# Optimization experiments

Measured on AMD Instinct MI355X. Metric: run time of the kernel, lower is better.

The kernel has to match this reference:

```python
import jax, jax.numpy as jnp
import numpy as np
from jax import lax

LEVELS = 3
K = 8  # db4 filter length
DEC_LO = jnp.asarray([-0.0105974018, 0.0328830117, 0.0308413818, -0.1870348117,
                      -0.0279837694, 0.6308807679, 0.7148465706, 0.2303778133], dtype=jnp.float32)
DEC_HI = jnp.asarray([-0.2303778133, 0.7148465706, -0.6308807679, -0.0279837694,
                      0.1870348117, 0.0308413818, -0.0328830117, -0.0105974018], dtype=jnp.float32)
REC_LO = jnp.asarray([0.2303778133, 0.7148465706, 0.6308807679, -0.0279837694,
                      -0.1870348117, 0.0308413818, 0.0328830117, -0.0105974018], dtype=jnp.float32)
REC_HI = jnp.asarray([-0.0105974018, -0.0328830117, 0.0308413818, 0.1870348117,
                      -0.0279837694, -0.6308807679, 0.7148465706, -0.2303778133], dtype=jnp.float32)
DN = ('NCH', 'OIH', 'NCH')


def _dwconv_stride2(x, w):
    # depthwise conv1d, stride 2, symmetric (reflect) pad of K-1 on both sides.
    # Same filter for every channel -> fold channels into batch for a single-filter conv.
    B, C, L = x.shape
    xp = jnp.pad(x, ((0, 0), (0, 0), (K - 1, K - 1)), mode='reflect')
    out = lax.conv_general_dilated(xp.reshape(B * C, 1, -1), w.reshape(1, 1, K),
                                   window_strides=(2,), padding='VALID',
                                   dimension_numbers=DN)
    return out.reshape(B, C, -1)


def _dwconvT_stride2(x, w):
    # depthwise conv_transpose1d, stride 2 == lhs-dilated conv with flipped kernel,
    # padding K-1 on both sides. Output length = 2*L + K - 2 (matches torch).
    B, C, L = x.shape
    out = lax.conv_general_dilated(x.reshape(B * C, 1, L), w[::-1].reshape(1, 1, K),
                                   window_strides=(1,), padding=[(K - 1, K - 1)],
                                   lhs_dilation=(2,), dimension_numbers=DN)
    return out.reshape(B, C, -1)


def _fit(out, target_len):
    # center-crop if too long, right-zero-pad if too short (as in torch code)
    L = out.shape[-1]
    if L > target_len:
        s = (L - target_len) // 2
        return out[..., s:s + target_len]
    if L < target_len:
        return jnp.pad(out, ((0, 0), (0, 0), (0, target_len - L)))
    return out


def setup_inputs() -> dict:
    key = jax.random.key(0)
    x = jax.random.normal(key, (16, 128, 8192), dtype=jnp.float32)
    return {"x": x}


def reference(x):
    # Multi-level analysis
    approx = x
    details = []
    target_lens = []
    for _ in range(LEVELS):
        target_lens.append(approx.shape[-1])
        details.append(_dwconv_stride2(approx, DEC_HI))
        approx = _dwconv_stride2(approx, DEC_LO)
    L0 = x.shape[-1]

    # Single-band reconstructions. Convolutions of the zero-filled bands in the
    # original torch code contribute exactly zero, so they are skipped here
    # (same math, fewer ops).
    def recon(band_idx):
        if band_idx == 0:  # approximation band: lo-path all the way up
            rec = approx
            for lvl in reversed(range(LEVELS)):
                rec = _fit(_dwconvT_stride2(rec, REC_LO), target_lens[lvl])
            return rec
        pick = LEVELS - band_idx  # which detail level to keep
        rec = _fit(_dwconvT_stride2(details[pick], REC_HI), target_lens[pick])
        for lvl in reversed(range(pick)):
            rec = _fit(_dwconvT_stride2(rec, REC_LO), target_lens[lvl])
        return rec

    bands = [_fit(recon(i), L0) for i in range(LEVELS + 1)]
    return jnp.stack(bands, axis=0)  # [LEVELS+1, B, C, L]
```

## Files before the change

### kernel.cpp

```cpp
#include <hip/hip_runtime.h>
#include <hip/hip_bf16.h>

#define NT 256

namespace {

constexpr int kL0 = 8192;
constexpr int kL1 = 4100;
constexpr int kL2 = 2054;
constexpr int kL3 = 1031;
constexpr int kRows = 16 * 128;

__constant__ __device__ const float kLO[8] = {-0.0105974018f, 0.0328830117f, 0.0308413818f, -0.1870348117f,
                                              -0.0279837694f, 0.6308807679f, 0.7148465706f, 0.2303778133f};
__constant__ __device__ const float kHI[8] = {-0.2303778133f, 0.7148465706f, -0.6308807679f, -0.0279837694f,
                                              0.1870348117f, 0.0308413818f, -0.0328830117f, -0.0105974018f};

__device__ __forceinline__ void analysis2(const float* __restrict__ s, int L, int Lo,
                                          float* __restrict__ alo, float* __restrict__ ahi)
{
  const int npairs = Lo >> 1;
  const int uHi = (L - 3) >> 2;
  for (int u = (int)threadIdx.x; u < npairs; u += NT) {
    if (u >= 2 && u <= uHi) {
      const float4* s4 = (const float4*)(s + 4 * u - 8);
      const float4 v0 = s4[0], v1 = s4[1], v2 = s4[2];
      const float w[10] = {v0.y, v0.z, v0.w, v1.x, v1.y, v1.z, v1.w, v2.x, v2.y, v2.z};
      float lo0 = 0.f, hi0 = 0.f, lo1 = 0.f, hi1 = 0.f;
#pragma unroll
      for (int k = 0; k < 8; ++k) {
        lo0 = fmaf(kLO[k], w[k], lo0);
        hi0 = fmaf(kHI[k], w[k], hi0);
        lo1 = fmaf(kLO[k], w[k + 2], lo1);
        hi1 = fmaf(kHI[k], w[k + 2], hi1);
      }
      ((float2*)alo)[u] = make_float2(lo0, lo1);
      ((float2*)ahi)[u] = make_float2(hi0, hi1);
    } else {
#pragma unroll
      for (int j = 0; j < 2; ++j) {
        const int i = 2 * u + j;
        const int base = 2 * i - 7;
        float slo = 0.f, shi = 0.f;
#pragma unroll
        for (int k = 0; k < 8; ++k) {
          int m = base + k;
          m = (m < 0) ? -m : m;
          m = (m >= L) ? (2 * L - 2 - m) : m;
          const float v = s[m];
          slo = fmaf(kLO[k], v, slo);
          shi = fmaf(kHI[k], v, shi);
        }
        alo[i] = slo;
        ahi[i] = shi;
      }
    }
  }
  if ((Lo & 1) && threadIdx.x == 0) {
    const int i = Lo - 1;
    const int base = 2 * i - 7;
    float slo = 0.f, shi = 0.f;
#pragma unroll
    for (int k = 0; k < 8; ++k) {
      int m = base + k;
      m = (m < 0) ? -m : m;
      m = (m >= L) ? (2 * L - 2 - m) : m;
      const float v = s[m];
      slo = fmaf(kLO[k], v, slo);
      shi = fmaf(kHI[k], v, shi);
    }
    alo[i] = slo;
    ahi[i] = shi;
  }
}

__device__ __forceinline__ void synthT4(const float* __restrict__ s, float* __restrict__ d, int T,
                                        float e0, float e1, float e2, float e3,
                                        float o0, float o1, float o2, float o3)
{
  const float2* __restrict__ s2 = (const float2*)s;
  const int nq = T >> 2;
  for (int t = (int)threadIdx.x; t < nq; t += NT) {
    const float2 p0 = s2[t];
    const float2 p1 = s2[t + 1];
    const float2 p2 = s2[t + 2];
    float4 r;
    r.x = fmaf(e3, p1.y, fmaf(e2, p1.x, fmaf(e1, p0.y, e0 * p0.x)));
    r.y = fmaf(o3, p2.x, fmaf(o2, p1.y, fmaf(o1, p1.x, o0 * p0.y)));
    r.z = fmaf(e3, p2.x, fmaf(e2, p1.y, fmaf(e1, p1.x, e0 * p0.y)));
    r.w = fmaf(o3, p2.y, fmaf(o2, p2.x, fmaf(o1, p1.y, o0 * p1.x)));
    ((float4*)d)[t] = r;
  }
  const int i0 = T & ~3;
  for (int i = i0 + (int)threadIdx.x; i < T; i += NT) {
    const int q = (i + 1) >> 1;
    const bool odd = (i & 1) != 0;
    const float c0 = odd ? o0 : e0;
    const float c1 = odd ? o1 : e1;
    const float c2 = odd ? o2 : e2;
    const float c3 = odd ? o3 : e3;
    float r = c0 * s[q];
    r = fmaf(c1, s[q + 1], r);
    r = fmaf(c2, s[q + 2], r);
    r = fmaf(c3, s[q + 3], r);
    d[i] = r;
  }
}

#define RL_E -0.0105974018f, 0.0308413818f, -0.0279837694f, 0.7148465706f
#define RL_O 0.0328830117f, -0.1870348117f, 0.6308807679f, 0.2303778133f
#define RH_E -0.2303778133f, -0.6308807679f, 0.1870348117f, -0.0328830117f
#define RH_O 0.7148465706f, -0.0279837694f, 0.0308413818f, -0.0105974018f

constexpr int kPool = 8224;

__global__ __launch_bounds__(NT, 4) void dwt_front(const float* __restrict__ x,
                                                   float* __restrict__ out)
{
  __shared__ float pool[kPool];
  const int row = blockIdx.x;
  const float* __restrict__ xr = x + (size_t)row * kL0;
  float* __restrict__ outr = out + (size_t)row * kL0;
  const size_t bs = (size_t)kRows * kL0;

  float* a1   = pool + 0;
  float* d1   = pool + 4104;
  float* a2   = pool + 4104;
  float* d2   = pool + 6160;
  float* t2b2 = pool + 0;
  float* a3   = pool + 0;
  float* d3   = pool + 1032;
  float* t1   = pool + 2064;
  float* t2   = pool + 4120;

  analysis2(xr, kL0, kL1, a1, d1);
  __syncthreads();
  synthT4(d1, outr + 3 * bs, kL0, RH_E, RH_O);
  __syncthreads();
  analysis2(a1, kL1, kL2, a2, d2);
  __syncthreads();
  synthT4(d2, t2b2, kL1, RH_E, RH_O);
  __syncthreads();
  synthT4(t2b2, outr + 2 * bs, kL0, RL_E, RL_O);
  __syncthreads();
  analysis2(a2, kL2, kL3, a3, d3);
  __syncthreads();
  synthT4(d3, t1, kL2, RH_E, RH_O);
  __syncthreads();
  synthT4(t1, t2, kL1, RL_E, RL_O);
  __syncthreads();
  synthT4(t2, outr + 1 * bs, kL0, RL_E, RL_O);
  __syncthreads();
  synthT4(a3, t1, kL2, RL_E, RL_O);
  __syncthreads();
  synthT4(t1, t2, kL1, RL_E, RL_O);
  __syncthreads();
  synthT4(t2, outr + 0 * bs, kL0, RL_E, RL_O);
}

}

extern "C" void kernel_launch(void* const* d_in, const int* in_sizes, int n_in,
                              void* d_out, int out_size, void* d_ws, size_t ws_size,
                              hipStream_t stream)
{
  const float* x = (const float*)d_in[0];
  float* out = (float*)d_out;
  dwt_front<<<dim3(kRows), dim3(NT), 0, stream>>>(x, out);
}
```

Measured before the change: 310.4 us.

## Split fused DWT kernel into analysis and per-band synthesis kernels

```diff
diff --git a/kernel.cpp b/kernel.cpp
--- a/kernel.cpp
+++ b/kernel.cpp
@@ -1,5 +1,4 @@
 #include <hip/hip_runtime.h>
-#include <hip/hip_bf16.h>
 
 #define NT 256
 
@@ -10,6 +9,12 @@
 constexpr int kL2 = 2054;
 constexpr int kL3 = 1031;
 constexpr int kRows = 16 * 128;
+
+constexpr int kWsD1 = 0;
+constexpr int kWsD2 = 4104;
+constexpr int kWsD3 = 6160;
+constexpr int kWsA3 = 7192;
+constexpr int kWsStride = 8224;
 
 __constant__ __device__ const float kLO[8] = {-0.0105974018f, 0.0328830117f, 0.0308413818f, -0.1870348117f,
                                               -0.0279837694f, 0.6308807679f, 0.7148465706f, 0.2303778133f};
@@ -112,50 +117,66 @@
 #define RH_E -0.2303778133f, -0.6308807679f, 0.1870348117f, -0.0328830117f
 #define RH_O 0.7148465706f, -0.0279837694f, 0.0308413818f, -0.0105974018f
 
-constexpr int kPool = 8224;
+__device__ __forceinline__ void stage4(const float* __restrict__ g, float* __restrict__ l, int n)
+{
+  const float4* g4 = (const float4*)g;
+  float4* l4 = (float4*)l;
+  const int nq = n >> 2;
+  for (int i = (int)threadIdx.x; i < nq; i += NT) l4[i] = g4[i];
+}
 
-__global__ __launch_bounds__(NT, 4) void dwt_front(const float* __restrict__ x,
+__global__ __launch_bounds__(NT, 4) void dwt_analysis(const float* __restrict__ x,
+                                                      float* __restrict__ ws)
+{
+  __shared__ __align__(16) float pool[6160];
+  const int row = blockIdx.x;
+  const float* __restrict__ xr = x + (size_t)row * kL0;
+  float* __restrict__ wr = ws + (size_t)row * kWsStride;
+
+  float* a1 = pool;
+  float* a2 = pool + 4104;
+
+  analysis2(xr, kL0, kL1, a1, wr + kWsD1);
+  __syncthreads();
+  analysis2(a1, kL1, kL2, a2, wr + kWsD2);
+  __syncthreads();
+  analysis2(a2, kL2, kL3, wr + kWsA3, wr + kWsD3);
+}
+
+__global__ __launch_bounds__(NT, 4) void dwt_synth(const float* __restrict__ ws,
                                                    float* __restrict__ out)
 {
-  __shared__ float pool[kPool];
-  const int row = blockIdx.x;
-  const float* __restrict__ xr = x + (size_t)row * kL0;
-  float* __restrict__ outr = out + (size_t)row * kL0;
-  const size_t bs = (size_t)kRows * kL0;
+  __shared__ __align__(16) float pool[6160];
+  const int bid = blockIdx.x;
+  const int row = bid >> 2;
+  const int band = bid & 3;
+  const float* __restrict__ wr = ws + (size_t)row * kWsStride;
+  float* __restrict__ outr = out + (size_t)band * (size_t)kRows * kL0 + (size_t)row * kL0;
 
-  float* a1   = pool + 0;
-  float* d1   = pool + 4104;
-  float* a2   = pool + 4104;
-  float* d2   = pool + 6160;
-  float* t2b2 = pool + 0;
-  float* a3   = pool + 0;
-  float* d3   = pool + 1032;
-  float* t1   = pool + 2064;
-  float* t2   = pool + 4120;
-
-  analysis2(xr, kL0, kL1, a1, d1);
-  __syncthreads();
-  synthT4(d1, outr + 3 * bs, kL0, RH_E, RH_O);
-  __syncthreads();
-  analysis2(a1, kL1, kL2, a2, d2);
-  __syncthreads();
-  synthT4(d2, t2b2, kL1, RH_E, RH_O);
-  __syncthreads();
-  synthT4(t2b2, outr + 2 * bs, kL0, RL_E, RL_O);
-  __syncthreads();
-  analysis2(a2, kL2, kL3, a3, d3);
-  __syncthreads();
-  synthT4(d3, t1, kL2, RH_E, RH_O);
-  __syncthreads();
-  synthT4(t1, t2, kL1, RL_E, RL_O);
-  __syncthreads();
-  synthT4(t2, outr + 1 * bs, kL0, RL_E, RL_O);
-  __syncthreads();
-  synthT4(a3, t1, kL2, RL_E, RL_O);
-  __syncthreads();
-  synthT4(t1, t2, kL1, RL_E, RL_O);
-  __syncthreads();
-  synthT4(t2, outr + 0 * bs, kL0, RL_E, RL_O);
+  if (band == 3) {
+    stage4(wr + kWsD1, pool, 4104);
+    __syncthreads();
+    synthT4(pool, outr, kL0, RH_E, RH_O);
+  } else if (band == 2) {
+    stage4(wr + kWsD2, pool + 4104, 2056);
+    __syncthreads();
+    synthT4(pool + 4104, pool, kL1, RH_E, RH_O);
+    __syncthreads();
+    synthT4(pool, outr, kL0, RL_E, RL_O);
+  } else {
+    const float* src = wr + (band == 1 ? kWsD3 : kWsA3);
+    stage4(src, pool, 1032);
+    __syncthreads();
+    if (band == 1) {
+      synthT4(pool, pool + 4104, kL2, RH_E, RH_O);
+    } else {
+      synthT4(pool, pool + 4104, kL2, RL_E, RL_O);
+    }
+    __syncthreads();
+    synthT4(pool + 4104, pool, kL1, RL_E, RL_O);
+    __syncthreads();
+    synthT4(pool, outr, kL0, RL_E, RL_O);
+  }
 }
 
 }
@@ -166,5 +187,7 @@
 {
   const float* x = (const float*)d_in[0];
   float* out = (float*)d_out;
-  dwt_front<<<dim3(kRows), dim3(NT), 0, stream>>>(x, out);
+  float* ws = (float*)d_ws;
+  dwt_analysis<<<dim3(kRows), dim3(NT), 0, stream>>>(x, ws);
+  dwt_synth<<<dim3(kRows * 4), dim3(NT), 0, stream>>>(ws, out);
 }
```

Result: slower. 356.3 us (+14.8%).

## Compose multi-level synthesis filters at compile time and fuse phases

Applied to the files above, without the earlier changes.

```diff
diff --git a/kernel.cpp b/kernel.cpp
--- a/kernel.cpp
+++ b/kernel.cpp
@@ -1,7 +1,6 @@
 #include <hip/hip_runtime.h>
-#include <hip/hip_bf16.h>
-
-#define NT 256
+
+#define NT 512
 
 namespace {
 
@@ -15,6 +14,51 @@
                                               -0.0279837694f, 0.6308807679f, 0.7148465706f, 0.2303778133f};
 __constant__ __device__ const float kHI[8] = {-0.2303778133f, 0.7148465706f, -0.6308807679f, -0.0279837694f,
                                               0.1870348117f, 0.0308413818f, -0.0328830117f, -0.0105974018f};
+
+constexpr float cRL[8] = {0.2303778133f, 0.7148465706f, 0.6308807679f, -0.0279837694f,
+                          -0.1870348117f, 0.0308413818f, 0.0328830117f, -0.0105974018f};
+constexpr float cRH[8] = {-0.0105974018f, -0.0328830117f, 0.0308413818f, 0.1870348117f,
+                          -0.0279837694f, -0.6308807679f, 0.7148465706f, -0.2303778133f};
+
+struct Tab2 { float c[4][6]; };
+struct Tab3 { float c[8][7]; };
+
+constexpr Tab2 compose2(const float (&w1)[8], const float (&w0)[8]) {
+  double acc[4][6] = {};
+  for (int r = 0; r < 4; ++r) {
+    const int i = 16 + r;
+    const int m0 = (i + 3) >> 2;
+    for (int j = (i + 1) / 2; j <= (i + 7) / 2; ++j) {
+      const double a = (double)w1[i + 7 - 2 * j];
+      for (int m = (j + 1) / 2; m <= (j + 7) / 2; ++m)
+        acc[r][m - m0] += a * (double)w0[j + 7 - 2 * m];
+    }
+  }
+  Tab2 T{};
+  for (int r = 0; r < 4; ++r)
+    for (int t = 0; t < 6; ++t) T.c[r][t] = (float)acc[r][t];
+  return T;
+}
+
+constexpr Tab3 compose3(const float (&w2)[8], const float (&w1)[8], const float (&w0)[8]) {
+  double acc[8][7] = {};
+  for (int r = 0; r < 8; ++r) {
+    const int i = 64 + r;
+    const int n0 = (i + 7) >> 3;
+    for (int j = (i + 1) / 2; j <= (i + 7) / 2; ++j) {
+      const double a = (double)w2[i + 7 - 2 * j];
+      for (int m = (j + 1) / 2; m <= (j + 7) / 2; ++m) {
+        const double b = a * (double)w1[j + 7 - 2 * m];
+        for (int n = (m + 1) / 2; n <= (m + 7) / 2; ++n)
+          acc[r][n - n0] += b * (double)w0[m + 7 - 2 * n];
+      }
+    }
+  }
+  Tab3 T{};
+  for (int r = 0; r < 8; ++r)
+    for (int t = 0; t < 7; ++t) T.c[r][t] = (float)acc[r][t];
+  return T;
+}
 
 __device__ __forceinline__ void analysis2(const float* __restrict__ s, int L, int Lo,
                                           float* __restrict__ alo, float* __restrict__ ahi)
@@ -91,71 +135,80 @@
     r.w = fmaf(o3, p2.y, fmaf(o2, p2.x, fmaf(o1, p1.y, o0 * p1.x)));
     ((float4*)d)[t] = r;
   }
-  const int i0 = T & ~3;
-  for (int i = i0 + (int)threadIdx.x; i < T; i += NT) {
-    const int q = (i + 1) >> 1;
-    const bool odd = (i & 1) != 0;
-    const float c0 = odd ? o0 : e0;
-    const float c1 = odd ? o1 : e1;
-    const float c2 = odd ? o2 : e2;
-    const float c3 = odd ? o3 : e3;
-    float r = c0 * s[q];
-    r = fmaf(c1, s[q + 1], r);
-    r = fmaf(c2, s[q + 2], r);
-    r = fmaf(c3, s[q + 3], r);
-    d[i] = r;
-  }
-}
-
-#define RL_E -0.0105974018f, 0.0308413818f, -0.0279837694f, 0.7148465706f
-#define RL_O 0.0328830117f, -0.1870348117f, 0.6308807679f, 0.2303778133f
+}
+
 #define RH_E -0.2303778133f, -0.6308807679f, 0.1870348117f, -0.0328830117f
 #define RH_O 0.7148465706f, -0.0279837694f, 0.0308413818f, -0.0105974018f
 
-constexpr int kPool = 8224;
-
-__global__ __launch_bounds__(NT, 4) void dwt_front(const float* __restrict__ x,
+__device__ __forceinline__ void synthC2(const float* __restrict__ s, float* __restrict__ d)
+{
+  constexpr Tab2 W = compose2(cRL, cRH);
+  for (int v = (int)threadIdx.x; v < (kL0 >> 2); v += NT) {
+    float w[7];
+#pragma unroll
+    for (int t = 0; t < 7; ++t) w[t] = s[v + t];
+    float r[4];
+#pragma unroll
+    for (int p = 0; p < 4; ++p) {
+      const int off = (p == 0) ? 0 : 1;
+      float acc = W.c[p][0] * w[off];
+#pragma unroll
+      for (int t = 1; t < 6; ++t) acc = fmaf(W.c[p][t], w[off + t], acc);
+      r[p] = acc;
+    }
+    ((float4*)d)[v] = make_float4(r[0], r[1], r[2], r[3]);
+  }
+}
+
+template <bool HI>
+__device__ __forceinline__ void synthC3(const float* __restrict__ s, float* __restrict__ d)
+{
+  constexpr Tab3 W = HI ? compose3(cRL, cRL, cRH) : compose3(cRL, cRL, cRL);
+  for (int v = (int)threadIdx.x; v < (kL0 >> 3); v += NT) {
+    float w[8];
+#pragma unroll
+    for (int t = 0; t < 8; ++t) w[t] = s[v + t];
+    float r[8];
+#pragma unroll
+    for (int p = 0; p < 8; ++p) {
+      const int off = (p == 0) ? 0 : 1;
+      float acc = W.c[p][0] * w[off];
+#pragma unroll
+      for (int t = 1; t < 7; ++t) acc = fmaf(W.c[p][t], w[off + t], acc);
+      r[p] = acc;
+    }
+    float4* d4 = (float4*)d;
+    d4[2 * v] = make_float4(r[0], r[1], r[2], r[3]);
+    d4[2 * v + 1] = make_float4(r[4], r[5], r[6], r[7]);
+  }
+}
+
+__global__ __launch_bounds__(NT, 6) void dwt_fused(const float* __restrict__ x,
                                                    float* __restrict__ out)
 {
-  __shared__ float pool[kPool];
+  __shared__ __align__(16) float pool[12320];
   const int row = blockIdx.x;
   const float* __restrict__ xr = x + (size_t)row * kL0;
   float* __restrict__ outr = out + (size_t)row * kL0;
   const size_t bs = (size_t)kRows * kL0;
 
-  float* a1   = pool + 0;
-  float* d1   = pool + 4104;
-  float* a2   = pool + 4104;
-  float* d2   = pool + 6160;
-  float* t2b2 = pool + 0;
-  float* a3   = pool + 0;
-  float* d3   = pool + 1032;
-  float* t1   = pool + 2064;
-  float* t2   = pool + 4120;
+  float* a1 = pool;
+  float* d1 = pool + 4104;
+  float* a2 = pool + 8208;
+  float* d2 = pool + 10264;
+  float* a3 = pool;
+  float* d3 = pool + 1032;
 
   analysis2(xr, kL0, kL1, a1, d1);
   __syncthreads();
+  analysis2(a1, kL1, kL2, a2, d2);
   synthT4(d1, outr + 3 * bs, kL0, RH_E, RH_O);
   __syncthreads();
-  analysis2(a1, kL1, kL2, a2, d2);
+  analysis2(a2, kL2, kL3, a3, d3);
+  synthC2(d2, outr + 2 * bs);
   __syncthreads();
-  synthT4(d2, t2b2, kL1, RH_E, RH_O);
-  __syncthreads();
-  synthT4(t2b2, outr + 2 * bs, kL0, RL_E, RL_O);
-  __syncthreads();
-  analysis2(a2, kL2, kL3, a3, d3);
-  __syncthreads();
-  synthT4(d3, t1, kL2, RH_E, RH_O);
-  __syncthreads();
-  synthT4(t1, t2, kL1, RL_E, RL_O);
-  __syncthreads();
-  synthT4(t2, outr + 1 * bs, kL0, RL_E, RL_O);
-  __syncthreads();
-  synthT4(a3, t1, kL2, RL_E, RL_O);
-  __syncthreads();
-  synthT4(t1, t2, kL1, RL_E, RL_O);
-  __syncthreads();
-  synthT4(t2, outr + 0 * bs, kL0, RL_E, RL_O);
+  synthC3<true>(d3, outr + 1 * bs);
+  synthC3<false>(a3, outr + 0 * bs);
 }
 
 }
@@ -166,5 +219,5 @@
 {
   const float* x = (const float*)d_in[0];
   float* out = (float*)d_out;
-  dwt_front<<<dim3(kRows), dim3(NT), 0, stream>>>(x, out);
-}
+  dwt_fused<<<dim3(kRows), dim3(NT), 0, stream>>>(x, out);
+}
```

Measured after the change: 319.5 us. +2.9%, slower.
